# Optimization experiments

Hardware: AMD Instinct MI355X
Metric: run time of the kernel (lower is better)

Reference implementation:

```python
import jax, jax.numpy as jnp
import numpy as np

H = 256; W = 256; N = 512
TANFOVX = 0.5; TANFOVY = 0.5
FX = W / (2.0 * TANFOVX)   # focal_x
FY = H / (2.0 * TANFOVY)   # focal_y


def _quat_to_rot(q):
    # q: [N,4] (w,x,y,z), normalized inside
    q = q / jnp.linalg.norm(q, axis=-1, keepdims=True)
    r, x, y, z = q[:, 0], q[:, 1], q[:, 2], q[:, 3]
    R = jnp.stack([
        1 - 2 * (y * y + z * z), 2 * (x * y - r * z), 2 * (x * z + r * y),
        2 * (x * y + r * z), 1 - 2 * (x * x + z * z), 2 * (y * z - r * x),
        2 * (x * z - r * y), 2 * (y * z + r * x), 1 - 2 * (x * x + y * y)],
        axis=-1).reshape(-1, 3, 3)
    return R


def _camera():
    # row-vector convention: t = [p,1] @ V ; full proj = V @ Pclip (3DGS style)
    V = np.eye(4, dtype=np.float32)
    V[3, :3] = [0.0, 0.0, 5.0]            # camera 5 units back along -z
    zn, zf = 0.01, 100.0
    P = np.zeros((4, 4), np.float32)
    P[0, 0] = 1.0 / TANFOVX
    P[1, 1] = 1.0 / TANFOVY
    P[2, 2] = zf / (zf - zn)
    P[3, 2] = -zf * zn / (zf - zn)
    P[2, 3] = 1.0
    return jnp.asarray(V), jnp.asarray(V @ P)


def setup_inputs() -> dict:
    key = jax.random.key(0)
    ks = jax.random.split(key, 5)
    means3D = jax.random.normal(ks[0], (N, 3), jnp.float32)
    opacities = jax.random.uniform(ks[1], (N, 1), jnp.float32)
    colors_precomp = jax.random.uniform(ks[2], (N, 3), jnp.float32)
    scales = 0.05 * jax.random.uniform(ks[3], (N, 3), jnp.float32) + 0.01
    rotations = jax.random.normal(ks[4], (N, 4), jnp.float32)
    viewmatrix, projmatrix = _camera()
    return dict(means3D=means3D, opacities=opacities,
                colors_precomp=colors_precomp, scales=scales,
                rotations=rotations, bg=jnp.zeros((3,), jnp.float32),
                viewmatrix=viewmatrix, projmatrix=projmatrix,
                campos=jnp.array([0.0, 0.0, -5.0], jnp.float32))


def _rasterize(means3D, opacities, colors, scales, rotations, bg,
               viewmatrix, projmatrix):
    n = means3D.shape[0]
    # --- 3D covariance: Sigma = (R S)(R S)^T ---
    Rm = _quat_to_rot(rotations)
    M = Rm * scales[:, None, :]                       # [N,3,3]
    Sigma = jnp.einsum('nij,nkj->nik', M, M)
    # --- camera-space positions ---
    ph = jnp.concatenate([means3D, jnp.ones((n, 1), means3D.dtype)], axis=1)
    t = ph @ viewmatrix                               # [N,4]
    tz = t[:, 2]
    tzc = jnp.maximum(tz, 1e-4)
    limx, limy = 1.3 * TANFOVX, 1.3 * TANFOVY
    txc = jnp.clip(t[:, 0] / tzc, -limx, limx) * tzc
    tyc = jnp.clip(t[:, 1] / tzc, -limy, limy) * tzc
    # --- EWA 2D covariance ---
    z0 = jnp.zeros_like(tz)
    J = jnp.stack([
        jnp.stack([FX / tzc, z0, -FX * txc / (tzc * tzc)], axis=-1),
        jnp.stack([z0, FY / tzc, -FY * tyc / (tzc * tzc)], axis=-1)],
        axis=1)                                        # [N,2,3]
    Wc = viewmatrix[:3, :3].T                          # column-vector rotation
    T = jnp.einsum('nij,jk->nik', J, Wc)               # [N,2,3]
    cov2d = jnp.einsum('nij,njk,nlk->nil', T, Sigma, T)
    cov2d = cov2d + 0.3 * jnp.eye(2, dtype=cov2d.dtype)  # low-pass dilation
    c00, c01, c11 = cov2d[:, 0, 0], cov2d[:, 0, 1], cov2d[:, 1, 1]
    det = c00 * c11 - c01 * c01
    det_inv = 1.0 / jnp.where(det != 0, det, 1.0)
    A = c11 * det_inv; B = -c01 * det_inv; C = c00 * det_inv  # conic
    mid = 0.5 * (c00 + c11)
    lam = mid + jnp.sqrt(jnp.maximum(mid * mid - det, 0.1))
    visible = (det > 0) & (tz > 0.2)
    radii = jnp.where(visible, jnp.ceil(3.0 * jnp.sqrt(lam)), 0.0).astype(jnp.int32)
    # --- screen-space means (ndc2pix) ---
    phom = ph @ projmatrix
    pw = 1.0 / (phom[:, 3] + 1e-7)
    mx = ((phom[:, 0] * pw + 1.0) * W - 1.0) * 0.5
    my = ((phom[:, 1] * pw + 1.0) * H - 1.0) * 0.5
    # --- depth sort (front-to-back) ---
    order = jnp.argsort(tz)
    mx, my = mx[order], my[order]
    A_, B_, C_ = A[order], B[order], C[order]
    op = opacities[order, 0]
    vis = visible[order]
    cols = colors[order]
    zs = tz[order]
    # --- per-pixel Gaussian evaluation [P, N] ---
    xs = jnp.arange(W, dtype=means3D.dtype)
    ys = jnp.arange(H, dtype=means3D.dtype)
    pix_x = jnp.tile(xs, H)
    pix_y = jnp.repeat(ys, W)
    dx = mx[None, :] - pix_x[:, None]
    dy = my[None, :] - pix_y[:, None]
    power = -0.5 * (A_[None, :] * dx * dx + C_[None, :] * dy * dy) \
            - B_[None, :] * dx * dy
    alpha = jnp.minimum(0.99, op[None, :] * jnp.exp(power))
    valid = (power <= 0.0) & vis[None, :] & (alpha >= 1.0 / 255.0)
    alpha = jnp.where(valid, alpha, 0.0)
    # --- front-to-back alpha compositing ---
    cum = jnp.cumprod(1.0 - alpha, axis=1)
    Tprev = jnp.concatenate(
        [jnp.ones((alpha.shape[0], 1), alpha.dtype), cum[:, :-1]], axis=1)
    wgt = alpha * Tprev                               # [P,N]
    Tfinal = cum[:, -1]
    color = wgt @ cols + Tfinal[:, None] * bg[None, :]
    depth = wgt @ zs
    color = color.reshape(H, W, 3).transpose(2, 0, 1)  # [3,H,W]
    return color, depth.reshape(H, W), Tfinal.reshape(H, W), radii


def reference(means3D, opacities, colors_precomp, scales, rotations, bg,
              viewmatrix, projmatrix, campos):
    return _rasterize(means3D, opacities, colors_precomp, scales, rotations,
                      bg, viewmatrix, projmatrix)
```

## Files before the change

kernel.cpp:

```cpp
#include <hip/hip_runtime.h>
#include <hip/hip_fp16.h>
#include <math.h>

#define NG 512
#define WI 256
#define HI 256
#define FXc 256.0f
#define FYc 256.0f
#define P2MIN -7.9943534368588578f

#if __has_builtin(__builtin_amdgcn_exp2f)
#define EXP2F(x) __builtin_amdgcn_exp2f(x)
#else
#define EXP2F(x) exp2f(x)
#endif


__device__ __align__(16) float4 g_q0[NG];
__device__ __align__(16) float4 g_q1[NG];
__device__ __align__(16) float4 g_cw[NG];

__global__ __launch_bounds__(256) void gs_prep(
    const float* __restrict__ means,
    const float* __restrict__ opac,
    const float* __restrict__ cols,
    const float* __restrict__ scales,
    const float* __restrict__ rots,
    const float* __restrict__ Vm,
    const float* __restrict__ Pm,
    float* __restrict__ out)
{
    int g = blockIdx.x * 256 + threadIdx.x;

    float qr = rots[g*4+0], qx = rots[g*4+1], qy = rots[g*4+2], qz = rots[g*4+3];
    float inv = rsqrtf(qr*qr + qx*qx + qy*qy + qz*qz);
    qr *= inv; qx *= inv; qy *= inv; qz *= inv;
    float R00 = 1.f - 2.f*(qy*qy + qz*qz);
    float R01 = 2.f*(qx*qy - qr*qz);
    float R02 = 2.f*(qx*qz + qr*qy);
    float R10 = 2.f*(qx*qy + qr*qz);
    float R11 = 1.f - 2.f*(qx*qx + qz*qz);
    float R12 = 2.f*(qy*qz - qr*qx);
    float R20 = 2.f*(qx*qz - qr*qy);
    float R21 = 2.f*(qy*qz + qr*qx);
    float R22 = 1.f - 2.f*(qx*qx + qy*qy);

    float s0 = scales[g*3+0], s1 = scales[g*3+1], s2 = scales[g*3+2];
    float M00=R00*s0, M01=R01*s1, M02=R02*s2;
    float M10=R10*s0, M11=R11*s1, M12=R12*s2;
    float M20=R20*s0, M21=R21*s1, M22=R22*s2;

    float S00 = M00*M00 + M01*M01 + M02*M02;
    float S01 = M00*M10 + M01*M11 + M02*M12;
    float S02 = M00*M20 + M01*M21 + M02*M22;
    float S11 = M10*M10 + M11*M11 + M12*M12;
    float S12 = M10*M20 + M11*M21 + M12*M22;
    float S22 = M20*M20 + M21*M21 + M22*M22;

    float px = means[g*3+0], py = means[g*3+1], pz = means[g*3+2];
    float t0 = px*Vm[0] + py*Vm[4] + pz*Vm[8]  + Vm[12];
    float t1 = px*Vm[1] + py*Vm[5] + pz*Vm[9]  + Vm[13];
    float tz = px*Vm[2] + py*Vm[6] + pz*Vm[10] + Vm[14];
    float tzc = fmaxf(tz, 1e-4f);
    const float limx = 1.3f*0.5f, limy = 1.3f*0.5f;
    float txc = fminf(fmaxf(t0 / tzc, -limx), limx) * tzc;
    float tyc = fminf(fmaxf(t1 / tzc, -limy), limy) * tzc;

    float J00 = FXc / tzc;
    float J02 = -FXc * txc / (tzc * tzc);
    float J11 = FYc / tzc;
    float J12 = -FYc * tyc / (tzc * tzc);

    float Ta0 = J00*Vm[0] + J02*Vm[2];
    float Ta1 = J00*Vm[4] + J02*Vm[6];
    float Ta2 = J00*Vm[8] + J02*Vm[10];
    float Tb0 = J11*Vm[1] + J12*Vm[2];
    float Tb1 = J11*Vm[5] + J12*Vm[6];
    float Tb2 = J11*Vm[9] + J12*Vm[10];

    float u0 = Ta0*S00 + Ta1*S01 + Ta2*S02;
    float u1 = Ta0*S01 + Ta1*S11 + Ta2*S12;
    float u2 = Ta0*S02 + Ta1*S12 + Ta2*S22;
    float v0 = Tb0*S00 + Tb1*S01 + Tb2*S02;
    float v1 = Tb0*S01 + Tb1*S11 + Tb2*S12;
    float v2 = Tb0*S02 + Tb1*S12 + Tb2*S22;
    float c00 = u0*Ta0 + u1*Ta1 + u2*Ta2 + 0.3f;
    float c01 = u0*Tb0 + u1*Tb1 + u2*Tb2;
    float c11 = v0*Tb0 + v1*Tb1 + v2*Tb2 + 0.3f;

    float det = c00*c11 - c01*c01;
    float det_inv = 1.f / ((det != 0.f) ? det : 1.f);
    float Aa =  c11 * det_inv;
    float Bb = -c01 * det_inv;
    float Cc =  c00 * det_inv;

    float mid = 0.5f*(c00 + c11);
    float lam = mid + sqrtf(fmaxf(mid*mid - det, 0.1f));
    bool vis = (det > 0.f) && (tz > 0.2f);
    float radf = vis ? ceilf(3.f*sqrtf(lam)) : 0.f;

    float h0 = px*Pm[0] + py*Pm[4] + pz*Pm[8]  + Pm[12];
    float h1 = px*Pm[1] + py*Pm[5] + pz*Pm[9]  + Pm[13];
    float h3 = px*Pm[3] + py*Pm[7] + pz*Pm[11] + Pm[15];
    float pw = 1.f / (h3 + 1e-7f);
    float mx = ((h0*pw + 1.f)*WI - 1.f)*0.5f;
    float my = ((h1*pw + 1.f)*HI - 1.f)*0.5f;

    float opv = vis ? opac[g] : 0.f;

    const float L2E = 1.4426950408889634f;
    float A2 = -0.5f*L2E*Aa;
    float B2 = -L2E*Bb;
    float C2 = -0.5f*L2E*Cc;
    float lop = (opv > 0.f) ? log2f(opv) : -3.0e38f;

    float a  = 0.5f*L2E*Aa;
    float c  = 0.5f*L2E*Cc;
    float bq = L2E*Bb;
    float qmax  = (vis && opv > 0.f) ? (lop + 7.9943534368588578f) : -1.0f;
    float amarg = a - bq*bq/(4.f*c);
    float cmarg = c - bq*bq/(4.f*a);

    out[5*WI*HI + g] = radf;

    union { __half2 h; float f; } prg, pbt;
    prg.h = __halves2half2(__float2half_rn(cols[g*3+0]), __float2half_rn(cols[g*3+1]));
    pbt.h = __halves2half2(__float2half_rn(cols[g*3+2]), __float2half_rn(tz));

    g_q0[g] = make_float4(mx, my, A2, B2);
    g_q1[g] = make_float4(C2, lop, prg.f, pbt.f);
    g_cw[g] = make_float4(amarg, cmarg, qmax, tz);
}

__global__ __launch_bounds__(256) void gs_tile(
    const float* __restrict__ bg,
    float* __restrict__ out)
{
    __shared__ __align__(16) float4 us[NG*2];
    __shared__ __align__(16) float4 cs[NG*2];
    __shared__ float skey[NG];
    __shared__ int wtot[4];

    int tx   = threadIdx.x;
    int lane = tx & 63;
    int wv   = tx >> 6;
    int b    = blockIdx.x;
    int x0   = (b & 15) << 4;
    int y0   = (b >> 4) << 4;
    float fx0 = (float)x0, fx1 = (float)(x0 + 15);
    float fy0 = (float)y0, fy1 = (float)(y0 + 15);

    float4 a0 = g_q0[2*tx],   a1 = g_q0[2*tx+1];
    float4 b0 = g_q1[2*tx],   b1 = g_q1[2*tx+1];
    float4 c0 = g_cw[2*tx],   c1 = g_cw[2*tx+1];

    float dxm0 = fmaxf(0.f, fmaxf(fx0 - a0.x, a0.x - fx1) - 0.0625f);
    float dym0 = fmaxf(0.f, fmaxf(fy0 - a0.y, a0.y - fy1) - 0.0625f);
    float dxm1 = fmaxf(0.f, fmaxf(fx0 - a1.x, a1.x - fx1) - 0.0625f);
    float dym1 = fmaxf(0.f, fmaxf(fy0 - a1.y, a1.y - fy1) - 0.0625f);
    bool f0 = (c0.x*dxm0*dxm0 <= c0.z) && (c0.y*dym0*dym0 <= c0.z);
    bool f1 = (c1.x*dxm1*dxm1 <= c1.z) && (c1.y*dym1*dym1 <= c1.z);

    unsigned long long m0 = __ballot(f0);
    unsigned long long m1 = __ballot(f1);
    unsigned long long lt = (1ULL << lane) - 1ULL;
    int pre = __popcll(m0 & lt) + __popcll(m1 & lt);
    if (lane == 0) wtot[wv] = __popcll(m0) + __popcll(m1);
    __syncthreads();

    int base = 0, n = 0;
    #pragma unroll
    for (int w2 = 0; w2 < 4; ++w2) {
        int t = wtot[w2];
        base += (w2 < wv) ? t : 0;
        n += t;
    }

    int p0 = base + pre;
    if (f0) {
        us[p0*2+0] = a0;
        us[p0*2+1] = b0;
        skey[p0]   = c0.w;
    }
    if (f1) {
        int p1 = p0 + (f0 ? 1 : 0);
        us[p1*2+0] = a1;
        us[p1*2+1] = b1;
        skey[p1]   = c1.w;
    }
    __syncthreads();

    for (int s = tx; s < n; s += 256) {
        float k = skey[s];
        int rank = 0;
        for (int j = 0; j < n; ++j) {
            float o = skey[j];
            rank += (o < k) || ((o == k) && (j < s));
        }
        cs[2*rank+0] = us[2*s+0];
        cs[2*rank+1] = us[2*s+1];
    }
    __syncthreads();

    float pxf = (float)(x0 + (tx & 15));
    float pyf = (float)(y0 + (tx >> 4));
    float T = 1.f, cr = 0.f, cg = 0.f, cb = 0.f, dp = 0.f;
    for (int j = 0; j < n; ++j) {
        float4 a = cs[2*j+0];
        float4 q = cs[2*j+1];
        float dx = a.x - pxf;
        float dy = a.y - pyf;
        float p2 = fmaf(fmaf(a.z, dx, a.w*dy), dx, fmaf(q.x*dy, dy, q.y));
        float al = fminf(0.99f, EXP2F(p2));
        al = ((p2 <= q.y) && (p2 >= P2MIN)) ? al : 0.f;
        float w = al * T;
        union { float f; __half2 h; } urg, ubt;
        urg.f = q.z; ubt.f = q.w;
        cr = fmaf(w, __low2float(urg.h),  cr);
        cg = fmaf(w, __high2float(urg.h), cg);
        cb = fmaf(w, __low2float(ubt.h),  cb);
        dp = fmaf(w, __high2float(ubt.h), dp);
        T -= w;
        if (__all(T < 1e-4f)) break;
    }

    const int HW = WI * HI;
    int p = (y0 + (tx >> 4)) * WI + x0 + (tx & 15);
    out[p]        = cr + T * bg[0];
    out[HW+p]     = cg + T * bg[1];
    out[2*HW+p]   = cb + T * bg[2];
    out[3*HW+p]   = dp;
    out[4*HW+p]   = T;
}

extern "C" void kernel_launch(void* const* d_in, const int* in_sizes, int n_in,
                              void* d_out, int out_size, void* d_ws, size_t ws_size,
                              hipStream_t stream)
{
    const float* means  = (const float*)d_in[0];
    const float* opac   = (const float*)d_in[1];
    const float* cols   = (const float*)d_in[2];
    const float* scales = (const float*)d_in[3];
    const float* rots   = (const float*)d_in[4];
    const float* bg     = (const float*)d_in[5];
    const float* Vm     = (const float*)d_in[6];
    const float* Pm     = (const float*)d_in[7];

    float* out = (float*)d_out;

    hipLaunchKernelGGL(gs_prep, dim3(2), dim3(256), 0, stream,
                       means, opac, cols, scales, rots, Vm, Pm, out);
    hipLaunchKernelGGL(gs_tile, dim3(256), dim3(256), 0, stream,
                       bg, out);
}
```

Baseline: 75.72 us.

## Fuse preprocessing into tile kernel with conservative per-tile culling and recompute

Merges the two launches into one kernel. Two extra blocks write the radii, and each tile block culls Gaussians itself using a cheap conservative bound (Jacobian Frobenius norm times max scale). It then recomputes the full covariance and conic only for the Gaussians that survive. This removes one kernel launch and the global round trip, at the cost of redundant per-tile preprocessing and a looser cull that may keep more candidates per tile.

```diff
diff --git a/kernel.cpp b/kernel.cpp
--- a/kernel.cpp
+++ b/kernel.cpp
@@ -16,22 +16,19 @@
 #endif
 
 
-__device__ __align__(16) float4 g_q0[NG];
-__device__ __align__(16) float4 g_q1[NG];
-__device__ __align__(16) float4 g_cw[NG];
-
-__global__ __launch_bounds__(256) void gs_prep(
+struct GRec {
+    float mx, my, A2, B2, C2, lop, radf, rg, bt;
+};
+
+__device__ inline GRec gs_heavy(int g,
     const float* __restrict__ means,
     const float* __restrict__ opac,
     const float* __restrict__ cols,
     const float* __restrict__ scales,
     const float* __restrict__ rots,
     const float* __restrict__ Vm,
-    const float* __restrict__ Pm,
-    float* __restrict__ out)
+    const float* __restrict__ Pm)
 {
-    int g = blockIdx.x * 256 + threadIdx.x;
-
     float qr = rots[g*4+0], qx = rots[g*4+1], qy = rots[g*4+2], qz = rots[g*4+3];
     float inv = rsqrtf(qr*qr + qx*qx + qy*qy + qz*qz);
     qr *= inv; qx *= inv; qy *= inv; qz *= inv;
@@ -97,7 +94,6 @@
     float mid = 0.5f*(c00 + c11);
     float lam = mid + sqrtf(fmaxf(mid*mid - det, 0.1f));
     bool vis = (det > 0.f) && (tz > 0.2f);
-    float radf = vis ? ceilf(3.f*sqrtf(lam)) : 0.f;
 
     float h0 = px*Pm[0] + py*Pm[4] + pz*Pm[8]  + Pm[12];
     float h1 = px*Pm[1] + py*Pm[5] + pz*Pm[9]  + Pm[13];
@@ -109,60 +105,95 @@
     float opv = vis ? opac[g] : 0.f;
 
     const float L2E = 1.4426950408889634f;
-    float A2 = -0.5f*L2E*Aa;
-    float B2 = -L2E*Bb;
-    float C2 = -0.5f*L2E*Cc;
-    float lop = (opv > 0.f) ? log2f(opv) : -3.0e38f;
-
-    float a  = 0.5f*L2E*Aa;
-    float c  = 0.5f*L2E*Cc;
-    float bq = L2E*Bb;
-    float qmax  = (vis && opv > 0.f) ? (lop + 7.9943534368588578f) : -1.0f;
-    float amarg = a - bq*bq/(4.f*c);
-    float cmarg = c - bq*bq/(4.f*a);
-
-    out[5*WI*HI + g] = radf;
+    GRec r;
+    r.mx = mx; r.my = my;
+    r.A2 = -0.5f*L2E*Aa;
+    r.B2 = -L2E*Bb;
+    r.C2 = -0.5f*L2E*Cc;
+    r.lop = (opv > 0.f) ? log2f(opv) : -3.0e38f;
+    r.radf = vis ? ceilf(3.f*sqrtf(lam)) : 0.f;
 
     union { __half2 h; float f; } prg, pbt;
     prg.h = __halves2half2(__float2half_rn(cols[g*3+0]), __float2half_rn(cols[g*3+1]));
     pbt.h = __halves2half2(__float2half_rn(cols[g*3+2]), __float2half_rn(tz));
-
-    g_q0[g] = make_float4(mx, my, A2, B2);
-    g_q1[g] = make_float4(C2, lop, prg.f, pbt.f);
-    g_cw[g] = make_float4(amarg, cmarg, qmax, tz);
+    r.rg = prg.f; r.bt = pbt.f;
+    return r;
 }
 
-__global__ __launch_bounds__(256) void gs_tile(
+__global__ __launch_bounds__(256) void gs_all(
+    const float* __restrict__ means,
+    const float* __restrict__ opac,
+    const float* __restrict__ cols,
+    const float* __restrict__ scales,
+    const float* __restrict__ rots,
+    const float* __restrict__ Vm,
+    const float* __restrict__ Pm,
     const float* __restrict__ bg,
     float* __restrict__ out)
 {
+    int b  = blockIdx.x;
+    int tx = threadIdx.x;
+
+    if (b < 2) {
+        int g = b*256 + tx;
+        GRec r = gs_heavy(g, means, opac, cols, scales, rots, Vm, Pm);
+        out[5*WI*HI + g] = r.radf;
+        return;
+    }
+
     __shared__ __align__(16) float4 us[NG*2];
     __shared__ __align__(16) float4 cs[NG*2];
     __shared__ float skey[NG];
-    __shared__ int wtot[4];
-
-    int tx   = threadIdx.x;
+    __shared__ int   sidx[NG];
+    __shared__ int   wtot[4];
+
     int lane = tx & 63;
     int wv   = tx >> 6;
-    int b    = blockIdx.x;
-    int x0   = (b & 15) << 4;
-    int y0   = (b >> 4) << 4;
+    int tile = b - 2;
+    int x0   = (tile & 15) << 4;
+    int y0   = (tile >> 4) << 4;
     float fx0 = (float)x0, fx1 = (float)(x0 + 15);
     float fy0 = (float)y0, fy1 = (float)(y0 + 15);
 
-    float4 a0 = g_q0[2*tx],   a1 = g_q0[2*tx+1];
-    float4 b0 = g_q1[2*tx],   b1 = g_q1[2*tx+1];
-    float4 c0 = g_cw[2*tx],   c1 = g_cw[2*tx+1];
-
-    float dxm0 = fmaxf(0.f, fmaxf(fx0 - a0.x, a0.x - fx1) - 0.0625f);
-    float dym0 = fmaxf(0.f, fmaxf(fy0 - a0.y, a0.y - fy1) - 0.0625f);
-    float dxm1 = fmaxf(0.f, fmaxf(fx0 - a1.x, a1.x - fx1) - 0.0625f);
-    float dym1 = fmaxf(0.f, fmaxf(fy0 - a1.y, a1.y - fy1) - 0.0625f);
-    bool f0 = (c0.x*dxm0*dxm0 <= c0.z) && (c0.y*dym0*dym0 <= c0.z);
-    bool f1 = (c1.x*dxm1*dxm1 <= c1.z) && (c1.y*dym1*dym1 <= c1.z);
-
-    unsigned long long m0 = __ballot(f0);
-    unsigned long long m1 = __ballot(f1);
+    bool  fl[2];
+    float tzv[2];
+    #pragma unroll
+    for (int i = 0; i < 2; ++i) {
+        int g = 2*tx + i;
+        float px = means[g*3+0], py = means[g*3+1], pz = means[g*3+2];
+        float t0 = px*Vm[0] + py*Vm[4] + pz*Vm[8]  + Vm[12];
+        float t1 = px*Vm[1] + py*Vm[5] + pz*Vm[9]  + Vm[13];
+        float tz = px*Vm[2] + py*Vm[6] + pz*Vm[10] + Vm[14];
+        float tzc = fmaxf(tz, 1e-4f);
+        const float limx = 1.3f*0.5f, limy = 1.3f*0.5f;
+        float txc = fminf(fmaxf(t0 / tzc, -limx), limx) * tzc;
+        float tyc = fminf(fmaxf(t1 / tzc, -limy), limy) * tzc;
+        float J00 = FXc / tzc;
+        float J02 = -FXc * txc / (tzc * tzc);
+        float J11 = FYc / tzc;
+        float J12 = -FYc * tyc / (tzc * tzc);
+        float jf2 = J00*J00 + J02*J02 + J11*J11 + J12*J12;
+
+        float s0 = scales[g*3+0], s1 = scales[g*3+1], s2 = scales[g*3+2];
+        float smax = fmaxf(s0, fmaxf(s1, s2));
+        float lam_ub = jf2*smax*smax + 0.3f;
+        float rad = 3.34f*sqrtf(lam_ub) + 0.125f;
+
+        float h0 = px*Pm[0] + py*Pm[4] + pz*Pm[8]  + Pm[12];
+        float h1 = px*Pm[1] + py*Pm[5] + pz*Pm[9]  + Pm[13];
+        float h3 = px*Pm[3] + py*Pm[7] + pz*Pm[11] + Pm[15];
+        float pw = 1.f / (h3 + 1e-7f);
+        float mx = ((h0*pw + 1.f)*WI - 1.f)*0.5f;
+        float my = ((h1*pw + 1.f)*HI - 1.f)*0.5f;
+
+        float dxm = fmaxf(0.f, fmaxf(fx0 - mx, mx - fx1));
+        float dym = fmaxf(0.f, fmaxf(fy0 - my, my - fy1));
+        fl[i]  = (tz > 0.2f) && (dxm*dxm + dym*dym <= rad*rad);
+        tzv[i] = tz;
+    }
+
+    unsigned long long m0 = __ballot(fl[0]);
+    unsigned long long m1 = __ballot(fl[1]);
     unsigned long long lt = (1ULL << lane) - 1ULL;
     int pre = __popcll(m0 & lt) + __popcll(m1 & lt);
     if (lane == 0) wtot[wv] = __popcll(m0) + __popcll(m1);
@@ -177,16 +208,22 @@
     }
 
     int p0 = base + pre;
-    if (f0) {
-        us[p0*2+0] = a0;
-        us[p0*2+1] = b0;
-        skey[p0]   = c0.w;
-    }
-    if (f1) {
-        int p1 = p0 + (f0 ? 1 : 0);
-        us[p1*2+0] = a1;
-        us[p1*2+1] = b1;
-        skey[p1]   = c1.w;
+    if (fl[0]) {
+        sidx[p0] = 2*tx;
+        skey[p0] = tzv[0];
+    }
+    if (fl[1]) {
+        int p1 = p0 + (fl[0] ? 1 : 0);
+        sidx[p1] = 2*tx + 1;
+        skey[p1] = tzv[1];
+    }
+    __syncthreads();
+
+    for (int s = tx; s < n; s += 256) {
+        int g = sidx[s];
+        GRec r = gs_heavy(g, means, opac, cols, scales, rots, Vm, Pm);
+        us[2*s+0] = make_float4(r.mx, r.my, r.A2, r.B2);
+        us[2*s+1] = make_float4(r.C2, r.lop, r.rg, r.bt);
     }
     __syncthreads();
 
@@ -248,8 +285,6 @@
 
     float* out = (float*)d_out;
 
-    hipLaunchKernelGGL(gs_prep, dim3(2), dim3(256), 0, stream,
-                       means, opac, cols, scales, rots, Vm, Pm, out);
-    hipLaunchKernelGGL(gs_tile, dim3(256), dim3(256), 0, stream,
-                       bg, out);
+    hipLaunchKernelGGL(gs_all, dim3(258), dim3(256), 0, stream,
+                       means, opac, cols, scales, rots, Vm, Pm, bg, out);
 }
```

New measurement: 76.63 us. About the same (+1.2%).
